# Kernel tuning notes

Hardware: AMD Instinct MI355X
Metric: run time of the kernel (lower is better)

The kernel has to match this reference:

```python
import math
import jax, jax.numpy as jnp
import numpy as np

B, S, D, H = 2, 2048, 2048, 16
HD = D // H  # 128


def _rope_tables(seq_len, head_dim, theta=10000.0):
    freqs = 1.0 / (theta ** (np.arange(0, head_dim, 2, dtype=np.float32) / head_dim))
    t = np.arange(seq_len, dtype=np.float32)
    ang = np.outer(t, freqs)  # [S, HD/2]
    return jnp.asarray(np.cos(ang)), jnp.asarray(np.sin(ang))


def setup_inputs() -> dict:
    key = jax.random.key(0)
    ks = jax.random.split(key, 5)
    sc = 1.0 / math.sqrt(D)
    x = jax.random.normal(ks[0], (B, S, D), dtype=jnp.float32)
    wq = jax.random.normal(ks[1], (D, D), dtype=jnp.float32) * sc
    wk = jax.random.normal(ks[2], (D, D), dtype=jnp.float32) * sc
    wv = jax.random.normal(ks[3], (D, D), dtype=jnp.float32) * sc
    wo = jax.random.normal(ks[4], (D, D), dtype=jnp.float32) * sc
    freqs_cos, freqs_sin = _rope_tables(S, HD)
    # additive causal mask: 0 on/below diagonal, -inf above
    mask = jnp.where(jnp.tril(jnp.ones((S, S), dtype=bool)), 0.0, -jnp.inf).astype(jnp.float32)
    return {"x": x, "wq": wq, "wk": wk, "wv": wv, "wo": wo,
            "freqs_cos": freqs_cos, "freqs_sin": freqs_sin,
            "mask": mask, "start_pos": 0}


def _apply_rope(t, cos, sin):
    # t: [B, S, H, HD]; pairs (even, odd) rotated as complex numbers (LLaMA style)
    tr = t.reshape(*t.shape[:-1], HD // 2, 2)
    te, to = tr[..., 0], tr[..., 1]
    c = cos[None, :, None, :]
    s = sin[None, :, None, :]
    out_e = te * c - to * s
    out_o = te * s + to * c
    return jnp.stack([out_e, out_o], axis=-1).reshape(t.shape)


def reference(x, wq, wk, wv, wo, freqs_cos, freqs_sin, mask, start_pos):
    bsz, seqlen, _ = x.shape
    xq = (x @ wq.T).reshape(bsz, seqlen, H, HD)
    xk = (x @ wk.T).reshape(bsz, seqlen, H, HD)
    xv = (x @ wv.T).reshape(bsz, seqlen, H, HD)
    xq = _apply_rope(xq, freqs_cos, freqs_sin)
    xk = _apply_rope(xk, freqs_cos, freqs_sin)
    # n_rep == 1 so repeat_kv is identity
    scores = jnp.einsum('bqhd,bkhd->bhqk', xq, xk) / math.sqrt(HD)
    scores = scores + mask  # broadcast [S,S] over [B,H,S,S]
    probs = jax.nn.softmax(scores.astype(jnp.float32), axis=-1).astype(xq.dtype)
    out = jnp.einsum('bhqk,bkhd->bqhd', probs, xv).reshape(bsz, seqlen, -1)
    return out @ wo.T
```

## Files before the change

### kernel.cpp

```cpp
#include <hip/hip_runtime.h>


typedef __bf16 bf16_t;
typedef __bf16 bf16x4 __attribute__((ext_vector_type(4)));
typedef __bf16 bf16x8 __attribute__((ext_vector_type(8)));
typedef float  f32x4  __attribute__((ext_vector_type(4)));

#define DEV __device__ __forceinline__

DEV void async_copy16(const bf16_t* g, bf16_t* lds_uniform_base) {
    __builtin_amdgcn_global_load_lds(
        (const __attribute__((address_space(1))) void*)g,
        (__attribute__((address_space(3))) void*)lds_uniform_base,
        16, 0, 0);
}

__global__ void cast_all(const float* __restrict__ x,  const float* __restrict__ wq,
                         const float* __restrict__ wk, const float* __restrict__ wv,
                         const float* __restrict__ wo,
                         bf16_t* __restrict__ xb, bf16_t* __restrict__ W3,
                         bf16_t* __restrict__ wob)
{
    const int i = blockIdx.x * blockDim.x + threadIdx.x;
    const float4* src;
    bf16x4* dst;
    if (i < 2097152) {
        src = (const float4*)x + i;
        dst = (bf16x4*)xb + i;
    } else {
        const int j   = i - 2097152;
        const int r   = j >> 20;
        const int off = j & 1048575;
        const float* s4 = (r == 0) ? wq : (r == 1) ? wk : (r == 2) ? wv : wo;
        src = (const float4*)s4 + off;
        dst = (r < 3) ? ((bf16x4*)W3 + (long)r * 1048576 + off)
                      : ((bf16x4*)wob + off);
    }
    const float4 v = *src;
    bf16x4 o = { (bf16_t)v.x, (bf16_t)v.y, (bf16_t)v.z, (bf16_t)v.w };
    *dst = o;
}

__global__ __launch_bounds__(256)
void gemm_qkv(const bf16_t* __restrict__ A, const bf16_t* __restrict__ Bm,
              bf16_t* __restrict__ Qo, bf16_t* __restrict__ Ko,
              bf16_t* __restrict__ VTo,
              const float* __restrict__ cosT, const float* __restrict__ sinT)
{
    constexpr int K = 2048;
    __shared__ bf16_t As[128 * 64];
    __shared__ bf16_t Bs[128 * 64];

    const int tid  = threadIdx.x;
    const int w    = tid >> 6;
    const int lane = tid & 63;
    const int l16  = lane & 15;
    const int quad = lane >> 4;
    const int l7   = l16 & 7;
    const int wm   = w >> 1, wn = w & 1;

    const int id   = blockIdx.x;
    const int xcd  = id & 7;
    const int slot = id >> 3;
    const int nl   = slot % 6;
    const int ml   = slot / 6;
    const long n0  = (long)(xcd * 6 + nl) * 128;
    const long m0  = (long)ml * 128;

    f32x4 acc[4][4] = {};

    const bf16_t* Ag[4];
    const bf16_t* Bg[4];
    #pragma unroll
    for (int i = 0; i < 4; ++i) {
        const int c   = i * 256 + tid;
        const int row = c >> 3;
        const int col = ((c & 7) ^ (row & 7)) * 8;
        Ag[i] = A  + (m0 + row) * K + col;
        Bg[i] = Bm + (n0 + row) * K + col;
    }

    for (int k0 = 0; k0 < K; k0 += 64) {
        __syncthreads();
        #pragma unroll
        for (int i = 0; i < 4; ++i) {
            async_copy16(Ag[i] + k0, As + i * 2048 + w * 512);
            async_copy16(Bg[i] + k0, Bs + i * 2048 + w * 512);
        }
        __syncthreads();

        #pragma unroll
        for (int kc = 0; kc < 2; ++kc) {
            bf16x8 af[4], bfr[4];
            #pragma unroll
            for (int t = 0; t < 4; ++t) {
                const int cs = ((kc * 4 + quad) ^ l7) * 8;
                af[t]  = *(const bf16x8*)&As[(wm * 64 + t * 16 + l16) * 64 + cs];
                bfr[t] = *(const bf16x8*)&Bs[(wn * 64 + t * 16 + l16) * 64 + cs];
            }
            #pragma unroll
            for (int mt = 0; mt < 4; ++mt)
                #pragma unroll
                for (int nt = 0; nt < 4; ++nt)
                    acc[mt][nt] = __builtin_amdgcn_mfma_f32_16x16x32_bf16(
                        af[mt], bfr[nt], acc[mt][nt], 0, 0, 0);
        }
    }

    const int region = (int)(n0 >> 11);
    #pragma unroll
    for (int mt = 0; mt < 4; ++mt) {
        #pragma unroll
        for (int nt = 0; nt < 4; ++nt) {
            if (region < 2) {
                bf16_t* dst = (region == 0) ? Qo : Ko;
                #pragma unroll
                for (int r = 0; r < 4; ++r) {
                    const long m = m0 + wm * 64 + mt * 16 + quad * 4 + r;
                    const long n = n0 + wn * 64 + nt * 16 + l16;
                    float v = acc[mt][nt][r];
                    const float partner = __shfl_xor(v, 1);
                    const int d    = (int)n & 127;
                    const int fidx = ((int)m & 2047) * 64 + (d >> 1);
                    const float c = cosT[fidx], s = sinT[fidx];
                    v = ((int)n & 1) ? fmaf(partner, s, v * c)
                                     : (v * c - partner * s);
                    dst[m * 2048 + (n & 2047)] = (bf16_t)v;
                }
            } else {
                const long m  = m0 + wm * 64 + mt * 16 + quad * 4;
                const int  np = (int)(n0 + wn * 64 + nt * 16 + l16) - 4096;
                bf16x4 pk;
                #pragma unroll
                for (int r = 0; r < 4; ++r) pk[r] = (bf16_t)acc[mt][nt][r];
                const int b  = (int)(m >> 11);
                const int s0 = (int)m & 2047;
                const long idx = ((long)(b * 16 + (np >> 7)) * 128 + (np & 127)) * 2048 + s0;
                *(bf16x4*)&VTo[idx] = pk;
            }
        }
    }
}

__global__ __launch_bounds__(256)
void gemm_out(const bf16_t* __restrict__ A, const bf16_t* __restrict__ Bm,
              float* __restrict__ Cp)
{
    constexpr int K = 2048, N = 2048;
    __shared__ bf16_t As[128 * 32];
    __shared__ bf16_t Bs[128 * 32];

    const int tid  = threadIdx.x;
    const int w    = tid >> 6;
    const int lane = tid & 63;
    const int l16  = lane & 15;
    const int quad = lane >> 4;
    const int wm   = w >> 1, wn = w & 1;

    const int id   = blockIdx.x;
    const int xcd  = id & 7;
    const int slot = id >> 3;
    const long n0  = (long)(xcd * 2 + (slot & 1)) * 128;
    const long m0  = (long)(slot >> 1) * 128;

    f32x4 acc[4][4] = {};

    const int srow = tid >> 2;
    const int soff = (tid & 3) * 8;
    const bf16_t* Ag = A  + (m0 + srow) * K + soff;
    const bf16_t* Bg = Bm + (n0 + srow) * K + soff;

    for (int k0 = 0; k0 < K; k0 += 32) {
        __syncthreads();
        async_copy16(Ag + k0,          As + w * 512);
        async_copy16(Ag + 64 * K + k0, As + 2048 + w * 512);
        async_copy16(Bg + k0,          Bs + w * 512);
        async_copy16(Bg + 64 * K + k0, Bs + 2048 + w * 512);
        __syncthreads();

        bf16x8 af[4], bfr[4];
        #pragma unroll
        for (int t = 0; t < 4; ++t) {
            af[t]  = *(const bf16x8*)&As[(wm * 64 + t * 16 + l16) * 32 + quad * 8];
            bfr[t] = *(const bf16x8*)&Bs[(wn * 64 + t * 16 + l16) * 32 + quad * 8];
        }
        #pragma unroll
        for (int mt = 0; mt < 4; ++mt)
            #pragma unroll
            for (int nt = 0; nt < 4; ++nt)
                acc[mt][nt] = __builtin_amdgcn_mfma_f32_16x16x32_bf16(
                    af[mt], bfr[nt], acc[mt][nt], 0, 0, 0);
    }

    #pragma unroll
    for (int mt = 0; mt < 4; ++mt)
        #pragma unroll
        for (int nt = 0; nt < 4; ++nt)
            #pragma unroll
            for (int r = 0; r < 4; ++r) {
                const long m = m0 + wm * 64 + mt * 16 + quad * 4 + r;
                const long n = n0 + wn * 64 + nt * 16 + l16;
                Cp[m * N + n] = acc[mt][nt][r];
            }
}

__global__ __launch_bounds__(256, 2)
void flash_attn(const bf16_t* __restrict__ Q, const bf16_t* __restrict__ Kg,
                const bf16_t* __restrict__ VT, bf16_t* __restrict__ O)
{
    constexpr int S = 2048, D = 2048;
    constexpr int PSTR = 72;
    __shared__ bf16_t Kb[2][64 * 128];
    __shared__ bf16_t Vb[2][128 * 64];
    __shared__ bf16_t Ps[128 * PSTR];

    const int tid  = threadIdx.x;
    const int w    = tid >> 6, lane = tid & 63, l16 = lane & 15, quad = lane >> 4;
    const int l7   = l16 & 7;

    const int id   = blockIdx.x;
    const int half = id >> 8;
    const int rest = id & 255;
    const int xcd  = rest & 7;
    const int s    = rest >> 3;
    const int hh   = s & 3;
    const int qh   = s >> 2;
    const int qt   = half ? (15 - qh) : qh;
    const int bh   = xcd * 4 + hh;
    const int b    = bh >> 4, h = bh & 15;
    const int q0   = qt * 128;

    bf16x8 qf[2][4];
    {
        const bf16_t* qp = Q + (long)(b * S + q0 + w * 32 + l16) * D + h * 128 + quad * 8;
        #pragma unroll
        for (int qi = 0; qi < 2; ++qi)
            #pragma unroll
            for (int kk = 0; kk < 4; ++kk)
                qf[qi][kk] = *(const bf16x8*)(qp + qi * 16 * D + kk * 32);
    }

    int koff[4], vof[4];
    #pragma unroll
    for (int i = 0; i < 4; ++i) {
        const int c  = i * 256 + tid;
        const int kr = c >> 4, cs = c & 15;
        const int cc = (cs & 8) | ((cs & 7) ^ (kr & 7));
        koff[i] = kr * D + cc * 8;
        const int d  = c >> 3, vs = c & 7;
        vof[i] = d * S + (vs ^ (d & 7)) * 8;
    }
    const bf16_t* Kst = Kg + (long)b * S * D + h * 128;
    const bf16_t* Vst = VT + (long)bh * 128 * S;

    f32x4 oacc[2][8] = {};
    float li[2] = { 0.f, 0.f };
    const float SC = 0.08838834764831845f * 1.44269504088896340f;

    const int nkt = 2 * qt + 2;

    #pragma unroll
    for (int i = 0; i < 4; ++i) {
        async_copy16(Kst + koff[i], &Kb[0][i * 2048 + w * 512]);
        async_copy16(Vst + vof[i], &Vb[0][i * 2048 + w * 512]);
    }

    for (int kt = 0; kt < nkt; ++kt) {
        __syncthreads();
        const int nk = (kt + 1 < nkt) ? kt + 1 : kt;
        #pragma unroll
        for (int i = 0; i < 4; ++i) {
            async_copy16(Kst + (long)nk * 64 * D + koff[i],
                         &Kb[(kt + 1) & 1][i * 2048 + w * 512]);
            async_copy16(Vst + (long)nk * 64 + vof[i],
                         &Vb[(kt + 1) & 1][i * 2048 + w * 512]);
        }

        const bool active = (kt * 64 <= q0 + w * 32 + 31);
        if (active) {
            f32x4 sc[4][2] = {};
            const bf16_t* Kcur = Kb[kt & 1];
            #pragma unroll
            for (int kk = 0; kk < 4; ++kk)
                #pragma unroll
                for (int mt = 0; mt < 4; ++mt) {
                    const int cc = kk * 4 + quad;
                    const bf16x8 kf = *(const bf16x8*)
                        &Kcur[(mt * 16 + l16) * 128 + ((cc & 8) | ((cc & 7) ^ l7)) * 8];
                    sc[mt][0] = __builtin_amdgcn_mfma_f32_16x16x32_bf16(
                        kf, qf[0][kk], sc[mt][0], 0, 0, 0);
                    sc[mt][1] = __builtin_amdgcn_mfma_f32_16x16x32_bf16(
                        kf, qf[1][kk], sc[mt][1], 0, 0, 0);
                }

            #pragma unroll
            for (int qi = 0; qi < 2; ++qi) {
                const int qg = q0 + w * 32 + qi * 16 + l16;
                float rs = 0.f;
                #pragma unroll
                for (int mt = 0; mt < 4; ++mt) {
                    bf16x4 pk;
                    #pragma unroll
                    for (int r = 0; r < 4; ++r) {
                        const int kg = kt * 64 + mt * 16 + quad * 4 + r;
                        const float p = (kg > qg) ? 0.f
                                      : exp2f(sc[mt][qi][r] * SC - 24.0f);
                        rs += p;
                        pk[r] = (bf16_t)p;
                    }
                    *(bf16x4*)&Ps[(w * 32 + qi * 16 + l16) * PSTR + mt * 16 + quad * 4] = pk;
                }
                li[qi] += rs;
            }

            const bf16_t* Vcur = Vb[kt & 1];
            #pragma unroll
            for (int ks = 0; ks < 2; ++ks) {
                const bf16x8 pf0 = *(const bf16x8*)
                    &Ps[(w * 32 + l16) * PSTR + ks * 32 + quad * 8];
                const bf16x8 pf1 = *(const bf16x8*)
                    &Ps[(w * 32 + 16 + l16) * PSTR + ks * 32 + quad * 8];
                #pragma unroll
                for (int nv = 0; nv < 8; ++nv) {
                    const bf16x8 vf = *(const bf16x8*)
                        &Vcur[(nv * 16 + l16) * 64 + ((ks * 4 + quad) ^ l7) * 8];
                    oacc[0][nv] = __builtin_amdgcn_mfma_f32_16x16x32_bf16(
                        pf0, vf, oacc[0][nv], 0, 0, 0);
                    oacc[1][nv] = __builtin_amdgcn_mfma_f32_16x16x32_bf16(
                        pf1, vf, oacc[1][nv], 0, 0, 0);
                }
            }
        }
    }

    #pragma unroll
    for (int qi = 0; qi < 2; ++qi) {
        li[qi] += __shfl_xor(li[qi], 16);
        li[qi] += __shfl_xor(li[qi], 32);
        const float inv = 1.0f / li[qi];
        #pragma unroll
        for (int r = 0; r < 4; ++r) {
            const float invr = __shfl(inv, quad * 4 + r);
            const long  row  = (long)(b * S + q0 + w * 32 + qi * 16 + quad * 4 + r);
            #pragma unroll
            for (int nv = 0; nv < 8; ++nv)
                O[row * D + h * 128 + nv * 16 + l16] = (bf16_t)(oacc[qi][nv][r] * invr);
        }
    }
}

extern "C" void kernel_launch(void* const* d_in, const int* in_sizes, int n_in,
                              void* d_out, int out_size, void* d_ws, size_t ws_size,
                              hipStream_t stream) {
    const float* x  = (const float*)d_in[0];
    const float* wq = (const float*)d_in[1];
    const float* wk = (const float*)d_in[2];
    const float* wv = (const float*)d_in[3];
    const float* wo = (const float*)d_in[4];
    const float* fc = (const float*)d_in[5];
    const float* fs = (const float*)d_in[6];

    char* ws = (char*)d_ws;
    bf16_t* xb  = (bf16_t*)(ws + 0);
    bf16_t* W3  = (bf16_t*)(ws + (16l << 20));
    bf16_t* wob = (bf16_t*)(ws + (40l << 20));
    bf16_t* Qb  = (bf16_t*)(ws + (48l << 20));
    bf16_t* Kb  = (bf16_t*)(ws + (64l << 20));
    bf16_t* VTb = (bf16_t*)(ws + (80l << 20));
    bf16_t* Ob  = xb;

    cast_all<<<24576, 256, 0, stream>>>(x, wq, wk, wv, wo, xb, W3, wob);

    gemm_qkv<<<1536, 256, 0, stream>>>(xb, W3, Qb, Kb, VTb, fc, fs);

    flash_attn<<<512, 256, 0, stream>>>(Qb, Kb, VTb, Ob);

    gemm_out<<<512, 256, 0, stream>>>(Ob, wob, (float*)d_out);
}
```

Baseline: 393.1 us.

## Rework QKV GEMM into 256x256 tiles with double-buffered LDS pipeline

The QKV projection GEMM moves from 128x128 tiles with 4 waves and a single LDS buffer to 256x256 tiles with 8 waves (512 threads). It adds a double-buffered LDS ping-pong schedule that interleaves async global-to-LDS loads with MFMA clusters, using explicit barriers, vmcnt/lgkmcnt waits and s_setprio around the MFMA bursts. The aim is to hide load latency and cut global traffic per FLOP through more reuse per tile. In exchange it uses 128KB of LDS per block, leaving at most one block per CU, and there are only 384 blocks, so occupancy and tail effects could offset the gains.

```diff
diff --git a/kernel.cpp b/kernel.cpp
--- a/kernel.cpp
+++ b/kernel.cpp
@@ -14,6 +14,12 @@
         (__attribute__((address_space(3))) void*)lds_uniform_base,
         16, 0, 0);
 }
+
+#define BAR    __builtin_amdgcn_s_barrier()
+#define LGKM0  asm volatile("s_waitcnt lgkmcnt(0)" ::: "memory")
+#define SP1    __builtin_amdgcn_s_setprio(1)
+#define SP0    __builtin_amdgcn_s_setprio(0)
+#define VMC(n) asm volatile("s_waitcnt vmcnt(" #n ")" ::: "memory")
 
 __global__ void cast_all(const float* __restrict__ x,  const float* __restrict__ wq,
                          const float* __restrict__ wk, const float* __restrict__ wv,
@@ -41,15 +47,15 @@
     *dst = o;
 }
 
-__global__ __launch_bounds__(256)
+__global__ __launch_bounds__(512, 2)
 void gemm_qkv(const bf16_t* __restrict__ A, const bf16_t* __restrict__ Bm,
               bf16_t* __restrict__ Qo, bf16_t* __restrict__ Ko,
               bf16_t* __restrict__ VTo,
               const float* __restrict__ cosT, const float* __restrict__ sinT)
 {
     constexpr int K = 2048;
-    __shared__ bf16_t As[128 * 64];
-    __shared__ bf16_t Bs[128 * 64];
+    __shared__ bf16_t As[2][16384];
+    __shared__ bf16_t Bs[2][16384];
 
     const int tid  = threadIdx.x;
     const int w    = tid >> 6;
@@ -57,66 +63,105 @@
     const int l16  = lane & 15;
     const int quad = lane >> 4;
     const int l7   = l16 & 7;
-    const int wm   = w >> 1, wn = w & 1;
+    const int wm   = w >> 2;
+    const int wn   = w & 3;
 
     const int id   = blockIdx.x;
     const int xcd  = id & 7;
     const int slot = id >> 3;
-    const int nl   = slot % 6;
-    const int ml   = slot / 6;
-    const long n0  = (long)(xcd * 6 + nl) * 128;
-    const long m0  = (long)ml * 128;
-
-    f32x4 acc[4][4] = {};
-
-    const bf16_t* Ag[4];
-    const bf16_t* Bg[4];
-    #pragma unroll
-    for (int i = 0; i < 4; ++i) {
-        const int c   = i * 256 + tid;
-        const int row = c >> 3;
-        const int col = ((c & 7) ^ (row & 7)) * 8;
-        Ag[i] = A  + (m0 + row) * K + col;
-        Bg[i] = Bm + (n0 + row) * K + col;
-    }
-
-    for (int k0 = 0; k0 < K; k0 += 64) {
-        __syncthreads();
-        #pragma unroll
-        for (int i = 0; i < 4; ++i) {
-            async_copy16(Ag[i] + k0, As + i * 2048 + w * 512);
-            async_copy16(Bg[i] + k0, Bs + i * 2048 + w * 512);
-        }
-        __syncthreads();
-
-        #pragma unroll
-        for (int kc = 0; kc < 2; ++kc) {
-            bf16x8 af[4], bfr[4];
-            #pragma unroll
-            for (int t = 0; t < 4; ++t) {
-                const int cs = ((kc * 4 + quad) ^ l7) * 8;
-                af[t]  = *(const bf16x8*)&As[(wm * 64 + t * 16 + l16) * 64 + cs];
-                bfr[t] = *(const bf16x8*)&Bs[(wn * 64 + t * 16 + l16) * 64 + cs];
-            }
-            #pragma unroll
-            for (int mt = 0; mt < 4; ++mt)
-                #pragma unroll
-                for (int nt = 0; nt < 4; ++nt)
-                    acc[mt][nt] = __builtin_amdgcn_mfma_f32_16x16x32_bf16(
-                        af[mt], bfr[nt], acc[mt][nt], 0, 0, 0);
-        }
-    }
+    const int nl   = slot % 3;
+    const int ml   = slot / 3;
+    const long n0  = (long)(xcd * 3 + nl) * 256;
+    const long m0  = (long)ml * 256;
+
+    f32x4 acc[8][4] = {};
+
+    const int  srow = w * 8 + (lane >> 3);
+    const int  scol = ((lane & 7) ^ ((lane >> 3) & 7)) * 8;
+    const long stg0 = (long)srow * K + scol;
+    const long stg1 = stg0 + 64l * K;
+
+    const bf16_t* Ab = A  + m0 * K;
+    const bf16_t* Bb = Bm + n0 * K;
+
+#define STG(gb, lb, h, kt) do {                                               \
+    const bf16_t* _g = (gb) + (long)(h) * 128 * K + (long)(kt) * 64;          \
+    async_copy16(_g + stg0, (lb) + (h) * 8192 + w * 512);                     \
+    async_copy16(_g + stg1, (lb) + (h) * 8192 + 4096 + w * 512);              \
+} while (0)
+
+#define RD_A4(bu, mb) { _Pragma("unroll") for (int kx = 0; kx < 2; ++kx)      \
+    _Pragma("unroll") for (int mx = 0; mx < 4; ++mx)                          \
+        ar[kx][mx] = *(const bf16x8*)&As[bu][                                 \
+            (wm * 128 + ((mb) + mx) * 16 + l16) * 64 +                        \
+            ((kx * 4 + quad) ^ l7) * 8]; }
+
+#define RD_B2(dstv, bu, nb) { _Pragma("unroll") for (int kx = 0; kx < 2; ++kx)\
+    _Pragma("unroll") for (int nx = 0; nx < 2; ++nx)                          \
+        dstv[kx][nx] = *(const bf16x8*)&Bs[bu][                               \
+            (wn * 64 + ((nb) + nx) * 16 + l16) * 64 +                         \
+            ((kx * 4 + quad) ^ l7) * 8]; }
+
+#define MFMA16(mb, bsrc, nb) { _Pragma("unroll") for (int mx = 0; mx < 4; ++mx)\
+    _Pragma("unroll") for (int nx = 0; nx < 2; ++nx)                          \
+    _Pragma("unroll") for (int kx = 0; kx < 2; ++kx)                          \
+        acc[(mb) + mx][(nb) + nx] = __builtin_amdgcn_mfma_f32_16x16x32_bf16(  \
+            ar[kx][mx], bsrc[kx][nx], acc[(mb) + mx][(nb) + nx], 0, 0, 0); }
+
+    bf16x8 ar[2][4], blo[2][2], bhi[2][2];
+
+    STG(Ab, As[0], 0, 0); STG(Ab, As[0], 1, 0);
+    STG(Bb, Bs[0], 0, 0); STG(Bb, Bs[0], 1, 0);
+    STG(Bb, Bs[1], 0, 1); STG(Bb, Bs[1], 1, 1);
+    VMC(4); BAR;
+
+    #pragma unroll 1
+    for (int it = 0; it < 16; ++it) {
+        const int t1 = 2 * it + 1;
+        const int t2 = (2 * it + 2 < 32) ? 2 * it + 2 : 31;
+        const int t3 = (2 * it + 3 < 32) ? 2 * it + 3 : 31;
+
+        RD_A4(0, 0); RD_B2(blo, 0, 0);
+        STG(Ab, As[1], 0, t1);
+        BAR; LGKM0; SP1; MFMA16(0, blo, 0); SP0; BAR;
+        RD_B2(bhi, 0, 2);
+        STG(Ab, As[1], 1, t1);
+        BAR; LGKM0; SP1; MFMA16(0, bhi, 2); SP0; BAR;
+        RD_A4(0, 4);
+        STG(Bb, Bs[0], 0, t2);
+        BAR; LGKM0; SP1; MFMA16(4, blo, 0); SP0; BAR;
+        STG(Bb, Bs[0], 1, t2);
+        BAR; LGKM0; SP1; MFMA16(4, bhi, 2); SP0; VMC(4); BAR;
+
+        RD_A4(1, 0); RD_B2(blo, 1, 0);
+        STG(Ab, As[0], 0, t2);
+        BAR; LGKM0; SP1; MFMA16(0, blo, 0); SP0; BAR;
+        RD_B2(bhi, 1, 2);
+        STG(Ab, As[0], 1, t2);
+        BAR; LGKM0; SP1; MFMA16(0, bhi, 2); SP0; BAR;
+        RD_A4(1, 4);
+        STG(Bb, Bs[1], 0, t3);
+        BAR; LGKM0; SP1; MFMA16(4, blo, 0); SP0; BAR;
+        STG(Bb, Bs[1], 1, t3);
+        BAR; LGKM0; SP1; MFMA16(4, bhi, 2); SP0; VMC(4); BAR;
+    }
+    VMC(0);
+
+#undef STG
+#undef RD_A4
+#undef RD_B2
+#undef MFMA16
 
     const int region = (int)(n0 >> 11);
     #pragma unroll
-    for (int mt = 0; mt < 4; ++mt) {
+    for (int mt = 0; mt < 8; ++mt) {
         #pragma unroll
         for (int nt = 0; nt < 4; ++nt) {
             if (region < 2) {
                 bf16_t* dst = (region == 0) ? Qo : Ko;
                 #pragma unroll
                 for (int r = 0; r < 4; ++r) {
-                    const long m = m0 + wm * 64 + mt * 16 + quad * 4 + r;
+                    const long m = m0 + wm * 128 + mt * 16 + quad * 4 + r;
                     const long n = n0 + wn * 64 + nt * 16 + l16;
                     float v = acc[mt][nt][r];
                     const float partner = __shfl_xor(v, 1);
@@ -128,7 +173,7 @@
                     dst[m * 2048 + (n & 2047)] = (bf16_t)v;
                 }
             } else {
-                const long m  = m0 + wm * 64 + mt * 16 + quad * 4;
+                const long m  = m0 + wm * 128 + mt * 16 + quad * 4;
                 const int  np = (int)(n0 + wn * 64 + nt * 16 + l16) - 4096;
                 bf16x4 pk;
                 #pragma unroll
@@ -371,7 +416,7 @@
 
     cast_all<<<24576, 256, 0, stream>>>(x, wq, wk, wv, wo, xb, W3, wob);
 
-    gemm_qkv<<<1536, 256, 0, stream>>>(xb, W3, Qb, Kb, VTb, fc, fs);
+    gemm_qkv<<<384, 512, 0, stream>>>(xb, W3, Qb, Kb, VTb, fc, fs);
 
     flash_attn<<<512, 256, 0, stream>>>(Qb, Kb, VTb, Ob);
 
```

After: 433.2 us. 1.1x slower.

## Double-buffer LDS tiles in QKV and output GEMMs, widen out-proj K tile

Applied to the files above, without the earlier changes.

Both GEMMs now hold two LDS buffers. The next K tile is prefetched with async global-to-LDS copies while MFMAs run on the current tile, which removes one barrier per iteration and overlaps load latency with compute. The output-projection GEMM also moves from a 32-wide to a 64-wide K tile with the same XOR-swizzled layout as the QKV GEMM, halving loop iterations and reducing LDS bank conflicts. In exchange, LDS per block rises to 64KB, which may limit how many blocks fit per CU.

```diff
diff --git a/kernel.cpp b/kernel.cpp
--- a/kernel.cpp
+++ b/kernel.cpp
@@ -48,8 +48,8 @@
               const float* __restrict__ cosT, const float* __restrict__ sinT)
 {
     constexpr int K = 2048;
-    __shared__ bf16_t As[128 * 64];
-    __shared__ bf16_t Bs[128 * 64];
+    __shared__ bf16_t As[2][8192];
+    __shared__ bf16_t Bs[2][8192];
 
     const int tid  = threadIdx.x;
     const int w    = tid >> 6;
@@ -80,14 +80,22 @@
         Bg[i] = Bm + (n0 + row) * K + col;
     }
 
+    #pragma unroll
+    for (int i = 0; i < 4; ++i) {
+        async_copy16(Ag[i], &As[0][i * 2048 + w * 512]);
+        async_copy16(Bg[i], &Bs[0][i * 2048 + w * 512]);
+    }
+
     for (int k0 = 0; k0 < K; k0 += 64) {
         __syncthreads();
-        #pragma unroll
-        for (int i = 0; i < 4; ++i) {
-            async_copy16(Ag[i] + k0, As + i * 2048 + w * 512);
-            async_copy16(Bg[i] + k0, Bs + i * 2048 + w * 512);
-        }
-        __syncthreads();
+        const int cur = (k0 >> 6) & 1;
+        if (k0 + 64 < K) {
+            #pragma unroll
+            for (int i = 0; i < 4; ++i) {
+                async_copy16(Ag[i] + k0 + 64, &As[cur ^ 1][i * 2048 + w * 512]);
+                async_copy16(Bg[i] + k0 + 64, &Bs[cur ^ 1][i * 2048 + w * 512]);
+            }
+        }
 
         #pragma unroll
         for (int kc = 0; kc < 2; ++kc) {
@@ -95,8 +103,8 @@
             #pragma unroll
             for (int t = 0; t < 4; ++t) {
                 const int cs = ((kc * 4 + quad) ^ l7) * 8;
-                af[t]  = *(const bf16x8*)&As[(wm * 64 + t * 16 + l16) * 64 + cs];
-                bfr[t] = *(const bf16x8*)&Bs[(wn * 64 + t * 16 + l16) * 64 + cs];
+                af[t]  = *(const bf16x8*)&As[cur][(wm * 64 + t * 16 + l16) * 64 + cs];
+                bfr[t] = *(const bf16x8*)&Bs[cur][(wn * 64 + t * 16 + l16) * 64 + cs];
             }
             #pragma unroll
             for (int mt = 0; mt < 4; ++mt)
@@ -147,14 +155,15 @@
               float* __restrict__ Cp)
 {
     constexpr int K = 2048, N = 2048;
-    __shared__ bf16_t As[128 * 32];
-    __shared__ bf16_t Bs[128 * 32];
+    __shared__ bf16_t As[2][8192];
+    __shared__ bf16_t Bs[2][8192];
 
     const int tid  = threadIdx.x;
     const int w    = tid >> 6;
     const int lane = tid & 63;
     const int l16  = lane & 15;
     const int quad = lane >> 4;
+    const int l7   = l16 & 7;
     const int wm   = w >> 1, wn = w & 1;
 
     const int id   = blockIdx.x;
@@ -165,31 +174,50 @@
 
     f32x4 acc[4][4] = {};
 
-    const int srow = tid >> 2;
-    const int soff = (tid & 3) * 8;
-    const bf16_t* Ag = A  + (m0 + srow) * K + soff;
-    const bf16_t* Bg = Bm + (n0 + srow) * K + soff;
-
-    for (int k0 = 0; k0 < K; k0 += 32) {
+    const bf16_t* Ag[4];
+    const bf16_t* Bg[4];
+    #pragma unroll
+    for (int i = 0; i < 4; ++i) {
+        const int c   = i * 256 + tid;
+        const int row = c >> 3;
+        const int col = ((c & 7) ^ (row & 7)) * 8;
+        Ag[i] = A  + (m0 + row) * K + col;
+        Bg[i] = Bm + (n0 + row) * K + col;
+    }
+
+    #pragma unroll
+    for (int i = 0; i < 4; ++i) {
+        async_copy16(Ag[i], &As[0][i * 2048 + w * 512]);
+        async_copy16(Bg[i], &Bs[0][i * 2048 + w * 512]);
+    }
+
+    for (int k0 = 0; k0 < K; k0 += 64) {
         __syncthreads();
-        async_copy16(Ag + k0,          As + w * 512);
-        async_copy16(Ag + 64 * K + k0, As + 2048 + w * 512);
-        async_copy16(Bg + k0,          Bs + w * 512);
-        async_copy16(Bg + 64 * K + k0, Bs + 2048 + w * 512);
-        __syncthreads();
-
-        bf16x8 af[4], bfr[4];
-        #pragma unroll
-        for (int t = 0; t < 4; ++t) {
-            af[t]  = *(const bf16x8*)&As[(wm * 64 + t * 16 + l16) * 32 + quad * 8];
-            bfr[t] = *(const bf16x8*)&Bs[(wn * 64 + t * 16 + l16) * 32 + quad * 8];
-        }
-        #pragma unroll
-        for (int mt = 0; mt < 4; ++mt)
-            #pragma unroll
-            for (int nt = 0; nt < 4; ++nt)
-                acc[mt][nt] = __builtin_amdgcn_mfma_f32_16x16x32_bf16(
-                    af[mt], bfr[nt], acc[mt][nt], 0, 0, 0);
+        const int cur = (k0 >> 6) & 1;
+        if (k0 + 64 < K) {
+            #pragma unroll
+            for (int i = 0; i < 4; ++i) {
+                async_copy16(Ag[i] + k0 + 64, &As[cur ^ 1][i * 2048 + w * 512]);
+                async_copy16(Bg[i] + k0 + 64, &Bs[cur ^ 1][i * 2048 + w * 512]);
+            }
+        }
+
+        #pragma unroll
+        for (int kc = 0; kc < 2; ++kc) {
+            bf16x8 af[4], bfr[4];
+            #pragma unroll
+            for (int t = 0; t < 4; ++t) {
+                const int cs = ((kc * 4 + quad) ^ l7) * 8;
+                af[t]  = *(const bf16x8*)&As[cur][(wm * 64 + t * 16 + l16) * 64 + cs];
+                bfr[t] = *(const bf16x8*)&Bs[cur][(wn * 64 + t * 16 + l16) * 64 + cs];
+            }
+            #pragma unroll
+            for (int mt = 0; mt < 4; ++mt)
+                #pragma unroll
+                for (int nt = 0; nt < 4; ++nt)
+                    acc[mt][nt] = __builtin_amdgcn_mfma_f32_16x16x32_bf16(
+                        af[mt], bfr[nt], acc[mt][nt], 0, 0, 0);
+        }
     }
 
     #pragma unroll
```

Measured after the change: 386.2 us. About the same (-1.7%).

## Add four-stage async LDS pipeline to GEMMs and swizzle attention P buffer

Applied to the files above, without the earlier changes.

Both projection GEMMs now use a 4-buffer ring in LDS with a K step of 32. Prefetches run three stages ahead, and each step uses a vmcnt wait plus a single barrier in place of the two __syncthreads per step. The GEMM LDS layout gets an XOR swizzle to avoid bank conflicts, and the attention P scratch drops its padded stride in favour of an XOR-swizzled 64-wide layout. The aim is to hide global load latency behind MFMA work, at the cost of more LDS per block (64KB), which may lower occupancy.

```diff
diff --git a/kernel.cpp b/kernel.cpp
--- a/kernel.cpp
+++ b/kernel.cpp
@@ -14,6 +14,9 @@
         (__attribute__((address_space(3))) void*)lds_uniform_base,
         16, 0, 0);
 }
+
+#define BAR    __builtin_amdgcn_s_barrier()
+#define VMC(n) asm volatile("s_waitcnt vmcnt(" #n ")" ::: "memory")
 
 __global__ void cast_all(const float* __restrict__ x,  const float* __restrict__ wq,
                          const float* __restrict__ wk, const float* __restrict__ wv,
@@ -48,15 +51,14 @@
               const float* __restrict__ cosT, const float* __restrict__ sinT)
 {
     constexpr int K = 2048;
-    __shared__ bf16_t As[128 * 64];
-    __shared__ bf16_t Bs[128 * 64];
+    __shared__ bf16_t As[4][4096];
+    __shared__ bf16_t Bs[4][4096];
 
     const int tid  = threadIdx.x;
     const int w    = tid >> 6;
     const int lane = tid & 63;
     const int l16  = lane & 15;
     const int quad = lane >> 4;
-    const int l7   = l16 & 7;
     const int wm   = w >> 1, wn = w & 1;
 
     const int id   = blockIdx.x;
@@ -69,43 +71,51 @@
 
     f32x4 acc[4][4] = {};
 
-    const bf16_t* Ag[4];
-    const bf16_t* Bg[4];
-    #pragma unroll
-    for (int i = 0; i < 4; ++i) {
+    const bf16_t* Ag[2];
+    const bf16_t* Bg[2];
+    #pragma unroll
+    for (int i = 0; i < 2; ++i) {
         const int c   = i * 256 + tid;
-        const int row = c >> 3;
-        const int col = ((c & 7) ^ (row & 7)) * 8;
+        const int row = c >> 2;
+        const int col = ((c & 3) ^ ((row >> 1) & 3)) * 8;
         Ag[i] = A  + (m0 + row) * K + col;
         Bg[i] = Bm + (n0 + row) * K + col;
     }
 
-    for (int k0 = 0; k0 < K; k0 += 64) {
-        __syncthreads();
-        #pragma unroll
-        for (int i = 0; i < 4; ++i) {
-            async_copy16(Ag[i] + k0, As + i * 2048 + w * 512);
-            async_copy16(Bg[i] + k0, Bs + i * 2048 + w * 512);
-        }
-        __syncthreads();
-
-        #pragma unroll
-        for (int kc = 0; kc < 2; ++kc) {
-            bf16x8 af[4], bfr[4];
-            #pragma unroll
-            for (int t = 0; t < 4; ++t) {
-                const int cs = ((kc * 4 + quad) ^ l7) * 8;
-                af[t]  = *(const bf16x8*)&As[(wm * 64 + t * 16 + l16) * 64 + cs];
-                bfr[t] = *(const bf16x8*)&Bs[(wn * 64 + t * 16 + l16) * 64 + cs];
-            }
-            #pragma unroll
-            for (int mt = 0; mt < 4; ++mt)
-                #pragma unroll
-                for (int nt = 0; nt < 4; ++nt)
-                    acc[mt][nt] = __builtin_amdgcn_mfma_f32_16x16x32_bf16(
-                        af[mt], bfr[nt], acc[mt][nt], 0, 0, 0);
-        }
-    }
+#define STAGE(t, bu) {                                                        \
+    _Pragma("unroll") for (int i = 0; i < 2; ++i) {                           \
+        async_copy16(Ag[i] + (t) * 32, &As[bu][i * 2048 + w * 512]);          \
+        async_copy16(Bg[i] + (t) * 32, &Bs[bu][i * 2048 + w * 512]);          \
+    } }
+
+    const int cs = (quad ^ ((l16 >> 1) & 3)) * 8;
+
+#define COMP(bu) {                                                            \
+    bf16x8 af[4], bfr[4];                                                     \
+    _Pragma("unroll") for (int t = 0; t < 4; ++t) {                           \
+        af[t]  = *(const bf16x8*)&As[bu][(wm * 64 + t * 16 + l16) * 32 + cs]; \
+        bfr[t] = *(const bf16x8*)&Bs[bu][(wn * 64 + t * 16 + l16) * 32 + cs]; \
+    }                                                                         \
+    _Pragma("unroll") for (int mt = 0; mt < 4; ++mt)                          \
+        _Pragma("unroll") for (int nt = 0; nt < 4; ++nt)                      \
+            acc[mt][nt] = __builtin_amdgcn_mfma_f32_16x16x32_bf16(            \
+                af[mt], bfr[nt], acc[mt][nt], 0, 0, 0); }
+
+    STAGE(0, 0); STAGE(1, 1); STAGE(2, 2);
+
+    #pragma unroll 1
+    for (int j = 0; j < 61; ++j) {
+        VMC(8);
+        BAR;
+        STAGE(j + 3, (j + 3) & 3);
+        COMP(j & 3);
+    }
+    VMC(8); BAR; COMP(1);
+    VMC(4); BAR; COMP(2);
+    VMC(0); BAR; COMP(3);
+
+#undef STAGE
+#undef COMP
 
     const int region = (int)(n0 >> 11);
     #pragma unroll
@@ -147,8 +157,8 @@
               float* __restrict__ Cp)
 {
     constexpr int K = 2048, N = 2048;
-    __shared__ bf16_t As[128 * 32];
-    __shared__ bf16_t Bs[128 * 32];
+    __shared__ bf16_t As[4][4096];
+    __shared__ bf16_t Bs[4][4096];
 
     const int tid  = threadIdx.x;
     const int w    = tid >> 6;
@@ -165,32 +175,51 @@
 
     f32x4 acc[4][4] = {};
 
-    const int srow = tid >> 2;
-    const int soff = (tid & 3) * 8;
-    const bf16_t* Ag = A  + (m0 + srow) * K + soff;
-    const bf16_t* Bg = Bm + (n0 + srow) * K + soff;
-
-    for (int k0 = 0; k0 < K; k0 += 32) {
-        __syncthreads();
-        async_copy16(Ag + k0,          As + w * 512);
-        async_copy16(Ag + 64 * K + k0, As + 2048 + w * 512);
-        async_copy16(Bg + k0,          Bs + w * 512);
-        async_copy16(Bg + 64 * K + k0, Bs + 2048 + w * 512);
-        __syncthreads();
-
-        bf16x8 af[4], bfr[4];
-        #pragma unroll
-        for (int t = 0; t < 4; ++t) {
-            af[t]  = *(const bf16x8*)&As[(wm * 64 + t * 16 + l16) * 32 + quad * 8];
-            bfr[t] = *(const bf16x8*)&Bs[(wn * 64 + t * 16 + l16) * 32 + quad * 8];
-        }
-        #pragma unroll
-        for (int mt = 0; mt < 4; ++mt)
-            #pragma unroll
-            for (int nt = 0; nt < 4; ++nt)
-                acc[mt][nt] = __builtin_amdgcn_mfma_f32_16x16x32_bf16(
-                    af[mt], bfr[nt], acc[mt][nt], 0, 0, 0);
-    }
+    const bf16_t* Ag[2];
+    const bf16_t* Bg[2];
+    #pragma unroll
+    for (int i = 0; i < 2; ++i) {
+        const int c   = i * 256 + tid;
+        const int row = c >> 2;
+        const int col = ((c & 3) ^ ((row >> 1) & 3)) * 8;
+        Ag[i] = A  + (m0 + row) * K + col;
+        Bg[i] = Bm + (n0 + row) * K + col;
+    }
+
+#define STAGE(t, bu) {                                                        \
+    _Pragma("unroll") for (int i = 0; i < 2; ++i) {                           \
+        async_copy16(Ag[i] + (t) * 32, &As[bu][i * 2048 + w * 512]);          \
+        async_copy16(Bg[i] + (t) * 32, &Bs[bu][i * 2048 + w * 512]);          \
+    } }
+
+    const int cs = (quad ^ ((l16 >> 1) & 3)) * 8;
+
+#define COMP(bu) {                                                            \
+    bf16x8 af[4], bfr[4];                                                     \
+    _Pragma("unroll") for (int t = 0; t < 4; ++t) {                           \
+        af[t]  = *(const bf16x8*)&As[bu][(wm * 64 + t * 16 + l16) * 32 + cs]; \
+        bfr[t] = *(const bf16x8*)&Bs[bu][(wn * 64 + t * 16 + l16) * 32 + cs]; \
+    }                                                                         \
+    _Pragma("unroll") for (int mt = 0; mt < 4; ++mt)                          \
+        _Pragma("unroll") for (int nt = 0; nt < 4; ++nt)                      \
+            acc[mt][nt] = __builtin_amdgcn_mfma_f32_16x16x32_bf16(            \
+                af[mt], bfr[nt], acc[mt][nt], 0, 0, 0); }
+
+    STAGE(0, 0); STAGE(1, 1); STAGE(2, 2);
+
+    #pragma unroll 1
+    for (int j = 0; j < 61; ++j) {
+        VMC(8);
+        BAR;
+        STAGE(j + 3, (j + 3) & 3);
+        COMP(j & 3);
+    }
+    VMC(8); BAR; COMP(1);
+    VMC(4); BAR; COMP(2);
+    VMC(0); BAR; COMP(3);
+
+#undef STAGE
+#undef COMP
 
     #pragma unroll
     for (int mt = 0; mt < 4; ++mt)
@@ -209,14 +238,14 @@
                 const bf16_t* __restrict__ VT, bf16_t* __restrict__ O)
 {
     constexpr int S = 2048, D = 2048;
-    constexpr int PSTR = 72;
     __shared__ bf16_t Kb[2][64 * 128];
     __shared__ bf16_t Vb[2][128 * 64];
-    __shared__ bf16_t Ps[128 * PSTR];
+    __shared__ bf16_t Ps[128 * 64];
 
     const int tid  = threadIdx.x;
     const int w    = tid >> 6, lane = tid & 63, l16 = lane & 15, quad = lane >> 4;
     const int l7   = l16 & 7;
+    const int rsw  = l16 & 12;
 
     const int id   = blockIdx.x;
     const int half = id >> 8;
@@ -296,6 +325,7 @@
             #pragma unroll
             for (int qi = 0; qi < 2; ++qi) {
                 const int qg = q0 + w * 32 + qi * 16 + l16;
+                const int prow = w * 32 + qi * 16 + l16;
                 float rs = 0.f;
                 #pragma unroll
                 for (int mt = 0; mt < 4; ++mt) {
@@ -308,7 +338,7 @@
                         rs += p;
                         pk[r] = (bf16_t)p;
                     }
-                    *(bf16x4*)&Ps[(w * 32 + qi * 16 + l16) * PSTR + mt * 16 + quad * 4] = pk;
+                    *(bf16x4*)&Ps[prow * 64 + ((mt * 4 + quad) ^ rsw) * 4] = pk;
                 }
                 li[qi] += rs;
             }
@@ -317,9 +347,9 @@
             #pragma unroll
             for (int ks = 0; ks < 2; ++ks) {
                 const bf16x8 pf0 = *(const bf16x8*)
-                    &Ps[(w * 32 + l16) * PSTR + ks * 32 + quad * 8];
+                    &Ps[(w * 32 + l16) * 64 + ((ks * 8 + quad * 2) ^ rsw) * 4];
                 const bf16x8 pf1 = *(const bf16x8*)
-                    &Ps[(w * 32 + 16 + l16) * PSTR + ks * 32 + quad * 8];
+                    &Ps[(w * 32 + 16 + l16) * 64 + ((ks * 8 + quad * 2) ^ rsw) * 4];
                 #pragma unroll
                 for (int nv = 0; nv < 8; ++nv) {
                     const bf16x8 vf = *(const bf16x8*)
```

After: 463.2 us. 1.18x slower.
